# Kernel optimization log

Measured on AMD Instinct MI355X. Metric: run time of the kernel, lower is better.

Reference implementation:

```python
import jax, jax.numpy as jnp
import numpy as np
import math

D_MODEL = 512
NUM_HEADS = 8
B, S = 2, 4096


def setup_inputs() -> dict:
    key = jax.random.key(0)
    ks = jax.random.split(key, 11)
    d = D_MODEL
    sc = 1.0 / math.sqrt(d)
    return {
        "query": jax.random.normal(ks[0], (B, S, d), jnp.float32),
        "key": jax.random.normal(ks[1], (B, S, d), jnp.float32),
        "value": jax.random.normal(ks[2], (B, S, d), jnp.float32),
        "Wq": jax.random.normal(ks[3], (d, d), jnp.float32) * sc,
        "bq": jnp.zeros((d,), jnp.float32),
        "Wk": jax.random.normal(ks[4], (d, d), jnp.float32) * sc,
        "bk": jnp.zeros((d,), jnp.float32),
        "Wv": jax.random.normal(ks[5], (d, d), jnp.float32) * sc,
        "bv": jnp.zeros((d,), jnp.float32),
        "Wo": jax.random.normal(ks[6], (d, d), jnp.float32) * sc,
        "bo": jnp.zeros((d,), jnp.float32),
    }


def reference(query, key, value, Wq, bq, Wk, bk, Wv, bv, Wo, bo):
    b, q_len, d_model = query.shape
    k_len = key.shape[1]
    h = NUM_HEADS
    d_k = d_model // h
    q = (query @ Wq.T + bq).reshape(b, q_len, h, d_k)
    k = (key @ Wk.T + bk).reshape(b, k_len, h, d_k)
    v = (value @ Wv.T + bv).reshape(b, k_len, h, d_k)
    # NOTE: faithful to source — softmax WITHOUT pre-scaling, then divide by sqrt(d_k)
    comp = jnp.einsum('bqhd,bkhd->bhqk', q, k)
    attn = jax.nn.softmax(comp, axis=-1) / jnp.sqrt(jnp.asarray(d_k, comp.dtype))
    x = jnp.einsum('bhqk,bkhd->bqhd', attn, v)
    return x.reshape(b, q_len, d_model) @ Wo.T + bo
```

## Files before the change

kernel.cpp:

```cpp
#include <hip/hip_runtime.h>

typedef _Float16 f16;
typedef __fp16 fp16x2 __attribute__((ext_vector_type(2)));
typedef _Float16 half4 __attribute__((ext_vector_type(4)));
typedef _Float16 half8 __attribute__((ext_vector_type(8)));
typedef float f32x4 __attribute__((ext_vector_type(4)));
typedef float float4v __attribute__((ext_vector_type(4)));
typedef float float2v __attribute__((ext_vector_type(2)));

#define LOG2E 1.44269504088896340736f

__device__ __forceinline__ half8 cat8(half4 a, half4 b) {
    half8 r;
    r[0] = a[0]; r[1] = a[1]; r[2] = a[2]; r[3] = a[3];
    r[4] = b[0]; r[5] = b[1]; r[6] = b[2]; r[7] = b[3];
    return r;
}

union H8 { fp16x2 h2[4]; half8 h8; };

#define TR8(baddr, d0,d1,d2,d3,d4,d5,d6,d7)                                   \
  asm volatile("ds_read_b64_tr_b16 %0, %8 offset:0\n\t"                       \
               "ds_read_b64_tr_b16 %1, %8 offset:512\n\t"                     \
               "ds_read_b64_tr_b16 %2, %8 offset:128\n\t"                     \
               "ds_read_b64_tr_b16 %3, %8 offset:640\n\t"                     \
               "ds_read_b64_tr_b16 %4, %8 offset:256\n\t"                     \
               "ds_read_b64_tr_b16 %5, %8 offset:768\n\t"                     \
               "ds_read_b64_tr_b16 %6, %8 offset:384\n\t"                     \
               "ds_read_b64_tr_b16 %7, %8 offset:896"                         \
               : "=&v"(d0),"=&v"(d1),"=&v"(d2),"=&v"(d3),                     \
                 "=&v"(d4),"=&v"(d5),"=&v"(d6),"=&v"(d7)                      \
               : "v"(baddr) : "memory")

#define LGKM0_FENCE()                                                          \
  do { asm volatile("s_waitcnt lgkmcnt(0)" ::: "memory");                      \
       __builtin_amdgcn_sched_barrier(0); } while (0)

__device__ __forceinline__ float rowmax16(const f32x4 sf[4]) {
    float a = fmaxf(fmaxf(sf[0][0], sf[0][1]), fmaxf(sf[0][2], sf[0][3]));
    float b = fmaxf(fmaxf(sf[1][0], sf[1][1]), fmaxf(sf[1][2], sf[1][3]));
    float c = fmaxf(fmaxf(sf[2][0], sf[2][1]), fmaxf(sf[2][2], sf[2][3]));
    float d = fmaxf(fmaxf(sf[3][0], sf[3][1]), fmaxf(sf[3][2], sf[3][3]));
    return fmaxf(fmaxf(a, b), fmaxf(c, d));
}

__device__ __forceinline__ void max_defer(
    const f32x4 sf[4], float& mL, f32x4 o[4], f32x4& la)
{
    float vm = rowmax16(sf);
    vm = fmaxf(vm, __shfl_xor(vm, 16, 64));
    vm = fmaxf(vm, __shfl_xor(vm, 32, 64));
    float vmL = vm * LOG2E;
    if (__any(vmL > mL + 8.0f)) {
        float mn = fmaxf(mL, vmL);
        float al = __builtin_amdgcn_exp2f(mL - mn);
        la *= al;
        #pragma unroll
        for (int db = 0; db < 4; ++db) o[db] *= al;
        mL = mn;
    }
}

__device__ __forceinline__ void exp_pack(
    const f32x4 sf[4], float mL, H8& pb0, H8& pb1)
{
    float pe[16];
    #pragma unroll
    for (int kb = 0; kb < 4; ++kb)
        #pragma unroll
        for (int ro = 0; ro < 4; ++ro)
            pe[kb * 4 + ro] = __builtin_amdgcn_exp2f(fmaf(sf[kb][ro], LOG2E, -mL));
    pb0.h2[0] = __builtin_amdgcn_cvt_pkrtz(pe[0],  pe[1]);
    pb0.h2[1] = __builtin_amdgcn_cvt_pkrtz(pe[2],  pe[3]);
    pb0.h2[2] = __builtin_amdgcn_cvt_pkrtz(pe[4],  pe[5]);
    pb0.h2[3] = __builtin_amdgcn_cvt_pkrtz(pe[6],  pe[7]);
    pb1.h2[0] = __builtin_amdgcn_cvt_pkrtz(pe[8],  pe[9]);
    pb1.h2[1] = __builtin_amdgcn_cvt_pkrtz(pe[10], pe[11]);
    pb1.h2[2] = __builtin_amdgcn_cvt_pkrtz(pe[12], pe[13]);
    pb1.h2[3] = __builtin_amdgcn_cvt_pkrtz(pe[14], pe[15]);
}

__global__ __launch_bounds__(256) void qkv_proj(
    const float* __restrict__ Aq, const float* __restrict__ Ak, const float* __restrict__ Av,
    const float* __restrict__ Wq, const float* __restrict__ Wk, const float* __restrict__ Wv,
    const float* __restrict__ bq, const float* __restrict__ bk, const float* __restrict__ bv,
    f16* __restrict__ Qh, f16* __restrict__ Kh, f16* __restrict__ Vh)
{
    const int z = blockIdx.z;
    const float* __restrict__ A    = (z == 0) ? Aq : (z == 1) ? Ak : Av;
    const float* __restrict__ W    = (z == 0) ? Wq : (z == 1) ? Wk : Wv;
    const float* __restrict__ bias = (z == 0) ? bq : (z == 1) ? bk : bv;
    f16* __restrict__ dst          = (z == 0) ? Qh : (z == 1) ? Kh : Vh;

    __shared__ __align__(16) f16 As[128 * 40];
    __shared__ __align__(16) f16 Ws[128 * 40];

    const int t  = threadIdx.x;
    const int m0 = blockIdx.y * 128;
    const int n0 = blockIdx.x * 128;
    const int w = t >> 6, lane = t & 63, lr = lane & 15, lg = lane >> 4;
    const int wr = w >> 1, wc = w & 1;

    f32x4 acc[4][4] = {};

    for (int k0 = 0; k0 < 512; k0 += 32) {
        #pragma unroll
        for (int it = 0; it < 2; ++it) {
            int c = t + it * 256;
            int row  = c >> 2;
            int col8 = (c & 3) * 8;

            const float* ga = A + (size_t)(m0 + row) * 512 + k0 + col8;
            float4v a0 = *(const float4v*)ga;
            float4v a1 = *(const float4v*)(ga + 4);
            half8 ha;
            ha[0] = (f16)a0[0]; ha[1] = (f16)a0[1]; ha[2] = (f16)a0[2]; ha[3] = (f16)a0[3];
            ha[4] = (f16)a1[0]; ha[5] = (f16)a1[1]; ha[6] = (f16)a1[2]; ha[7] = (f16)a1[3];
            *(half8*)&As[row * 40 + col8] = ha;

            const float* gw = W + (size_t)(n0 + row) * 512 + k0 + col8;
            float4v w0 = *(const float4v*)gw;
            float4v w1 = *(const float4v*)(gw + 4);
            half8 hw;
            hw[0] = (f16)w0[0]; hw[1] = (f16)w0[1]; hw[2] = (f16)w0[2]; hw[3] = (f16)w0[3];
            hw[4] = (f16)w1[0]; hw[5] = (f16)w1[1]; hw[6] = (f16)w1[2]; hw[7] = (f16)w1[3];
            *(half8*)&Ws[row * 40 + col8] = hw;
        }
        __syncthreads();

        half8 af[4], bf[4];
        #pragma unroll
        for (int i = 0; i < 4; ++i) {
            af[i] = *(const half8*)&As[(wr * 64 + i * 16 + lr) * 40 + lg * 8];
            bf[i] = *(const half8*)&Ws[(wc * 64 + i * 16 + lr) * 40 + lg * 8];
        }
        #pragma unroll
        for (int mi = 0; mi < 4; ++mi)
            #pragma unroll
            for (int ni = 0; ni < 4; ++ni)
                acc[mi][ni] = __builtin_amdgcn_mfma_f32_16x16x32_f16(af[mi], bf[ni], acc[mi][ni], 0, 0, 0);
        __syncthreads();
    }

    #pragma unroll
    for (int mi = 0; mi < 4; ++mi) {
        #pragma unroll
        for (int ni = 0; ni < 4; ++ni) {
            int col = n0 + wc * 64 + ni * 16 + lr;
            float bv_ = bias[col];
            int h  = col >> 6;
            int dd = col & 63;
            #pragma unroll
            for (int r = 0; r < 4; ++r) {
                int row = m0 + wr * 64 + mi * 16 + lg * 4 + r;
                int b = row >> 12;
                int s = row & 4095;
                dst[(((size_t)(b * 8 + h)) * 4096 + s) * 64 + dd] = (f16)(acc[mi][ni][r] + bv_);
            }
        }
    }
}

__global__ __launch_bounds__(256, 2) void flash_attn(
    const f16* __restrict__ Qh, const f16* __restrict__ Kh, const f16* __restrict__ Vh,
    f16* __restrict__ Xp, float2v* __restrict__ mlp)
{
    const int bh  = blockIdx.y;
    const int z   = blockIdx.z;
    const int t = threadIdx.x, w = t >> 6, lane = t & 63, lr = lane & 15, lg = lane >> 4;
    const int q0 = blockIdx.x * 128 + w * 32;

    __shared__ __align__(16) f16 Ks[2][64 * 72];
    __shared__ __align__(16) f16 Vs[2][64 * 64];

    const size_t hb = (size_t)bh * (4096 * 64);

    half8 aq00 = *(const half8*)&Qh[hb + (size_t)(q0 + lr) * 64 + lg * 8];
    half8 aq01 = *(const half8*)&Qh[hb + (size_t)(q0 + lr) * 64 + 32 + lg * 8];
    half8 aq10 = *(const half8*)&Qh[hb + (size_t)(q0 + 16 + lr) * 64 + lg * 8];
    half8 aq11 = *(const half8*)&Qh[hb + (size_t)(q0 + 16 + lr) * 64 + 32 + lg * 8];

    half8 ones;
    #pragma unroll
    for (int j = 0; j < 8; ++j) ones[j] = (f16)1.0f;
    const f32x4 zf = {0.0f, 0.0f, 0.0f, 0.0f};

    const int srow = t >> 3;
    const int scol = (t & 7) * 8;
    const int kdstA = srow * 72 + scol;
    const int kdstB = kdstA + 32 * 72;
    const int vdstA = ((((srow >> 2) & 3) * 16) + (srow >> 4) * 4 + (scol >> 4)) * 64
                    + (srow & 3) * 16 + (scol & 15);
    const int vdstB = vdstA + 512;

    f32x4 o0[4] = {}, o1[4] = {};
    f32x4 la0 = {}, la1 = {};
    float mL0 = -INFINITY, mL1 = -INFINITY;

    const f16* kbase = Kh + hb + (size_t)(z * 2048 + srow) * 64 + scol;
    const f16* vbase = Vh + hb + (size_t)(z * 2048 + srow) * 64 + scol;

    half8 kregA = *(const half8*)kbase;
    half8 kregB = *(const half8*)(kbase + 2048);
    half8 vregA = *(const half8*)vbase;
    half8 vregB = *(const half8*)(vbase + 2048);

    for (int kt = 0; kt < 2048; kt += 64) {
        const int bi = (kt >> 6) & 1;
        f16* ks = &Ks[bi][0];
        f16* vs = &Vs[bi][0];

        *(half8*)&ks[kdstA] = kregA;
        *(half8*)&ks[kdstB] = kregB;
        *(half8*)&vs[vdstA] = vregA;
        *(half8*)&vs[vdstB] = vregB;
        __syncthreads();

        int koff = ((kt + 64) & 2047) << 6;
        kregA = *(const half8*)(kbase + koff);
        kregB = *(const half8*)(kbase + 2048 + koff);
        vregA = *(const half8*)(vbase + koff);
        vregB = *(const half8*)(vbase + 2048 + koff);

        f32x4 sf0[4], sf1[4];
        {
            half8 kf[4];
            #pragma unroll
            for (int kb = 0; kb < 4; ++kb)
                kf[kb] = *(const half8*)&ks[(kb * 16 + lr) * 72 + lg * 8];
            __builtin_amdgcn_s_setprio(1);
            #pragma unroll
            for (int kb = 0; kb < 4; ++kb)
                sf0[kb] = __builtin_amdgcn_mfma_f32_16x16x32_f16(kf[kb], aq00, zf, 0, 0, 0);
            #pragma unroll
            for (int kb = 0; kb < 4; ++kb)
                sf1[kb] = __builtin_amdgcn_mfma_f32_16x16x32_f16(kf[kb], aq10, zf, 0, 0, 0);
            __builtin_amdgcn_s_setprio(0);
            #pragma unroll
            for (int kb = 0; kb < 4; ++kb)
                kf[kb] = *(const half8*)&ks[(kb * 16 + lr) * 72 + 32 + lg * 8];
            __builtin_amdgcn_s_setprio(1);
            #pragma unroll
            for (int kb = 0; kb < 4; ++kb)
                sf0[kb] = __builtin_amdgcn_mfma_f32_16x16x32_f16(kf[kb], aq01, sf0[kb], 0, 0, 0);
            #pragma unroll
            for (int kb = 0; kb < 4; ++kb)
                sf1[kb] = __builtin_amdgcn_mfma_f32_16x16x32_f16(kf[kb], aq11, sf1[kb], 0, 0, 0);
            __builtin_amdgcn_s_setprio(0);
        }

        max_defer(sf0, mL0, o0, la0);
        max_defer(sf1, mL1, o1, la1);

        const unsigned vb = (unsigned)(size_t)vs + (unsigned)(lg * 2048 + lr * 8);
        half4 ua0,ua1,ua2,ua3,ua4,ua5,ua6,ua7;
        half4 ub0,ub1,ub2,ub3,ub4,ub5,ub6,ub7;
        TR8(vb,         ua0,ua1,ua2,ua3,ua4,ua5,ua6,ua7);
        TR8(vb + 1024u, ub0,ub1,ub2,ub3,ub4,ub5,ub6,ub7);

        H8 p00, p01, p10, p11;
        exp_pack(sf0, mL0, p00, p01);
        exp_pack(sf1, mL1, p10, p11);

        LGKM0_FENCE();

        __builtin_amdgcn_s_setprio(1);
        o0[0] = __builtin_amdgcn_mfma_f32_16x16x32_f16(cat8(ua0,ua1), p00.h8, o0[0], 0, 0, 0);
        o0[1] = __builtin_amdgcn_mfma_f32_16x16x32_f16(cat8(ua2,ua3), p00.h8, o0[1], 0, 0, 0);
        o0[2] = __builtin_amdgcn_mfma_f32_16x16x32_f16(cat8(ua4,ua5), p00.h8, o0[2], 0, 0, 0);
        o0[3] = __builtin_amdgcn_mfma_f32_16x16x32_f16(cat8(ua6,ua7), p00.h8, o0[3], 0, 0, 0);
        o1[0] = __builtin_amdgcn_mfma_f32_16x16x32_f16(cat8(ua0,ua1), p10.h8, o1[0], 0, 0, 0);
        o1[1] = __builtin_amdgcn_mfma_f32_16x16x32_f16(cat8(ua2,ua3), p10.h8, o1[1], 0, 0, 0);
        o1[2] = __builtin_amdgcn_mfma_f32_16x16x32_f16(cat8(ua4,ua5), p10.h8, o1[2], 0, 0, 0);
        o1[3] = __builtin_amdgcn_mfma_f32_16x16x32_f16(cat8(ua6,ua7), p10.h8, o1[3], 0, 0, 0);
        la0 = __builtin_amdgcn_mfma_f32_16x16x32_f16(ones, p00.h8, la0, 0, 0, 0);
        la1 = __builtin_amdgcn_mfma_f32_16x16x32_f16(ones, p10.h8, la1, 0, 0, 0);
        o0[0] = __builtin_amdgcn_mfma_f32_16x16x32_f16(cat8(ub0,ub1), p01.h8, o0[0], 0, 0, 0);
        o0[1] = __builtin_amdgcn_mfma_f32_16x16x32_f16(cat8(ub2,ub3), p01.h8, o0[1], 0, 0, 0);
        o0[2] = __builtin_amdgcn_mfma_f32_16x16x32_f16(cat8(ub4,ub5), p01.h8, o0[2], 0, 0, 0);
        o0[3] = __builtin_amdgcn_mfma_f32_16x16x32_f16(cat8(ub6,ub7), p01.h8, o0[3], 0, 0, 0);
        o1[0] = __builtin_amdgcn_mfma_f32_16x16x32_f16(cat8(ub0,ub1), p11.h8, o1[0], 0, 0, 0);
        o1[1] = __builtin_amdgcn_mfma_f32_16x16x32_f16(cat8(ub2,ub3), p11.h8, o1[1], 0, 0, 0);
        o1[2] = __builtin_amdgcn_mfma_f32_16x16x32_f16(cat8(ub4,ub5), p11.h8, o1[2], 0, 0, 0);
        o1[3] = __builtin_amdgcn_mfma_f32_16x16x32_f16(cat8(ub6,ub7), p11.h8, o1[3], 0, 0, 0);
        la0 = __builtin_amdgcn_mfma_f32_16x16x32_f16(ones, p01.h8, la0, 0, 0, 0);
        la1 = __builtin_amdgcn_mfma_f32_16x16x32_f16(ones, p11.h8, la1, 0, 0, 0);
        __builtin_amdgcn_s_setprio(0);
    }

    const int b = bh >> 3, h = bh & 7;
    f16* X = Xp + (size_t)z * (8192 * 512);
    const float inv0 = 1.0f / la0[0];
    const float inv1 = 1.0f / la1[0];
    const int q0_ = q0 + lr, q1_ = q0 + 16 + lr;
    #pragma unroll
    for (int db = 0; db < 4; ++db) {
        half4 hv0, hv1;
        hv0[0] = (f16)(o0[db][0] * inv0);
        hv0[1] = (f16)(o0[db][1] * inv0);
        hv0[2] = (f16)(o0[db][2] * inv0);
        hv0[3] = (f16)(o0[db][3] * inv0);
        *(half4*)&X[((size_t)(b * 4096 + q0_)) * 512 + h * 64 + db * 16 + lg * 4] = hv0;
        hv1[0] = (f16)(o1[db][0] * inv1);
        hv1[1] = (f16)(o1[db][1] * inv1);
        hv1[2] = (f16)(o1[db][2] * inv1);
        hv1[3] = (f16)(o1[db][3] * inv1);
        *(half4*)&X[((size_t)(b * 4096 + q1_)) * 512 + h * 64 + db * 16 + lg * 4] = hv1;
    }

    if (lane < 16) {
        float2v m0v; m0v[0] = mL0; m0v[1] = la0[0];
        float2v m1v; m1v[0] = mL1; m1v[1] = la1[0];
        mlp[(size_t)z * 65536 + bh * 4096 + q0_] = m0v;
        mlp[(size_t)z * 65536 + bh * 4096 + q1_] = m1v;
    }
}

__global__ __launch_bounds__(256) void out_proj(
    const f16* __restrict__ Xp, const float2v* __restrict__ mlp,
    const float* __restrict__ Wo, const float* __restrict__ bo,
    float* __restrict__ out)
{
    __shared__ __align__(16) f16 As[128 * 40];
    __shared__ __align__(16) f16 Ws[128 * 40];

    const int t  = threadIdx.x;
    const int m0 = blockIdx.y * 128;
    const int n0 = blockIdx.x * 128;
    const int w = t >> 6, lane = t & 63, lr = lane & 15, lg = lane >> 4;
    const int wr = w >> 1, wc = w & 1;

    f32x4 acc[4][4] = {};

    for (int k0 = 0; k0 < 512; k0 += 32) {
        #pragma unroll
        for (int it = 0; it < 2; ++it) {
            int c = t + it * 256;
            int row  = c >> 2;
            int col8 = (c & 3) * 8;
            int gcol = k0 + col8;
            int tok  = m0 + row;

            int bhq = ((tok >> 12) * 8 + (gcol >> 6)) * 4096 + (tok & 4095);
            float2v ml1 = mlp[bhq];
            float2v ml2 = mlp[65536 + bhq];
            float mm = fmaxf(ml1[0], ml2[0]);
            float a1 = __builtin_amdgcn_exp2f(ml1[0] - mm) * ml1[1];
            float a2 = __builtin_amdgcn_exp2f(ml2[0] - mm) * ml2[1];
            float inv = 1.0f / (8.0f * (a1 + a2));
            float w1 = a1 * inv, w2 = a2 * inv;

            const size_t xoff = (size_t)tok * 512 + gcol;
            half8 x1 = *(const half8*)&Xp[xoff];
            half8 x2 = *(const half8*)&Xp[(size_t)8192 * 512 + xoff];
            half8 hx;
            #pragma unroll
            for (int j = 0; j < 8; ++j)
                hx[j] = (f16)(w1 * (float)x1[j] + w2 * (float)x2[j]);
            *(half8*)&As[row * 40 + col8] = hx;

            const float* gw = Wo + (size_t)(n0 + row) * 512 + k0 + col8;
            float4v w0 = *(const float4v*)gw;
            float4v w1v = *(const float4v*)(gw + 4);
            half8 hw;
            hw[0] = (f16)w0[0];  hw[1] = (f16)w0[1];  hw[2] = (f16)w0[2];  hw[3] = (f16)w0[3];
            hw[4] = (f16)w1v[0]; hw[5] = (f16)w1v[1]; hw[6] = (f16)w1v[2]; hw[7] = (f16)w1v[3];
            *(half8*)&Ws[row * 40 + col8] = hw;
        }
        __syncthreads();

        half8 af[4], bf[4];
        #pragma unroll
        for (int i = 0; i < 4; ++i) {
            af[i] = *(const half8*)&As[(wr * 64 + i * 16 + lr) * 40 + lg * 8];
            bf[i] = *(const half8*)&Ws[(wc * 64 + i * 16 + lr) * 40 + lg * 8];
        }
        #pragma unroll
        for (int mi = 0; mi < 4; ++mi)
            #pragma unroll
            for (int ni = 0; ni < 4; ++ni)
                acc[mi][ni] = __builtin_amdgcn_mfma_f32_16x16x32_f16(af[mi], bf[ni], acc[mi][ni], 0, 0, 0);
        __syncthreads();
    }

    #pragma unroll
    for (int mi = 0; mi < 4; ++mi) {
        #pragma unroll
        for (int ni = 0; ni < 4; ++ni) {
            int col = n0 + wc * 64 + ni * 16 + lr;
            float bb = bo[col];
            #pragma unroll
            for (int r = 0; r < 4; ++r) {
                int row = m0 + wr * 64 + mi * 16 + lg * 4 + r;
                out[(size_t)row * 512 + col] = acc[mi][ni][r] + bb;
            }
        }
    }
}

extern "C" void kernel_launch(void* const* d_in, const int* in_sizes, int n_in,
                              void* d_out, int out_size, void* d_ws, size_t ws_size,
                              hipStream_t stream) {
    const float* query = (const float*)d_in[0];
    const float* key   = (const float*)d_in[1];
    const float* value = (const float*)d_in[2];
    const float* Wq    = (const float*)d_in[3];
    const float* bq    = (const float*)d_in[4];
    const float* Wk    = (const float*)d_in[5];
    const float* bk    = (const float*)d_in[6];
    const float* Wv    = (const float*)d_in[7];
    const float* bv    = (const float*)d_in[8];
    const float* Wo    = (const float*)d_in[9];
    const float* bo    = (const float*)d_in[10];
    float* out = (float*)d_out;

    char* ws = (char*)d_ws;
    f16*     Qh  = (f16*)(ws);
    f16*     Kh  = (f16*)(ws + 8388608);
    f16*     Vh  = (f16*)(ws + 16777216);
    f16*     Xp  = (f16*)(ws + 25165824);
    float2v* mlp = (float2v*)(ws + 41943040);

    qkv_proj<<<dim3(4, 64, 3), 256, 0, stream>>>(query, key, value,
                                                 Wq, Wk, Wv, bq, bk, bv,
                                                 Qh, Kh, Vh);
    flash_attn<<<dim3(32, 16, 2), 256, 0, stream>>>(Qh, Kh, Vh, Xp, mlp);
    out_proj<<<dim3(4, 64), 256, 0, stream>>>(Xp, mlp, Wo, bo, out);
}
```

Before: 170.3 us.

## Store V transposed from projection and drop LDS transpose reads in attention

```diff
diff --git a/kernel.cpp b/kernel.cpp
--- a/kernel.cpp
+++ b/kernel.cpp
@@ -10,31 +10,8 @@
 
 #define LOG2E 1.44269504088896340736f
 
-__device__ __forceinline__ half8 cat8(half4 a, half4 b) {
-    half8 r;
-    r[0] = a[0]; r[1] = a[1]; r[2] = a[2]; r[3] = a[3];
-    r[4] = b[0]; r[5] = b[1]; r[6] = b[2]; r[7] = b[3];
-    return r;
-}
-
 union H8 { fp16x2 h2[4]; half8 h8; };
-
-#define TR8(baddr, d0,d1,d2,d3,d4,d5,d6,d7)                                   \
-  asm volatile("ds_read_b64_tr_b16 %0, %8 offset:0\n\t"                       \
-               "ds_read_b64_tr_b16 %1, %8 offset:512\n\t"                     \
-               "ds_read_b64_tr_b16 %2, %8 offset:128\n\t"                     \
-               "ds_read_b64_tr_b16 %3, %8 offset:640\n\t"                     \
-               "ds_read_b64_tr_b16 %4, %8 offset:256\n\t"                     \
-               "ds_read_b64_tr_b16 %5, %8 offset:768\n\t"                     \
-               "ds_read_b64_tr_b16 %6, %8 offset:384\n\t"                     \
-               "ds_read_b64_tr_b16 %7, %8 offset:896"                         \
-               : "=&v"(d0),"=&v"(d1),"=&v"(d2),"=&v"(d3),                     \
-                 "=&v"(d4),"=&v"(d5),"=&v"(d6),"=&v"(d7)                      \
-               : "v"(baddr) : "memory")
-
-#define LGKM0_FENCE()                                                          \
-  do { asm volatile("s_waitcnt lgkmcnt(0)" ::: "memory");                      \
-       __builtin_amdgcn_sched_barrier(0); } while (0)
+union HV { half8 h8; half4 h4[2]; };
 
 __device__ __forceinline__ float rowmax16(const f32x4 sf[4]) {
     float a = fmaxf(fmaxf(sf[0][0], sf[0][1]), fmaxf(sf[0][2], sf[0][3]));
@@ -84,13 +61,13 @@
     const float* __restrict__ Aq, const float* __restrict__ Ak, const float* __restrict__ Av,
     const float* __restrict__ Wq, const float* __restrict__ Wk, const float* __restrict__ Wv,
     const float* __restrict__ bq, const float* __restrict__ bk, const float* __restrict__ bv,
-    f16* __restrict__ Qh, f16* __restrict__ Kh, f16* __restrict__ Vh)
+    f16* __restrict__ Qh, f16* __restrict__ Kh, f16* __restrict__ Vt)
 {
     const int z = blockIdx.z;
     const float* __restrict__ A    = (z == 0) ? Aq : (z == 1) ? Ak : Av;
     const float* __restrict__ W    = (z == 0) ? Wq : (z == 1) ? Wk : Wv;
     const float* __restrict__ bias = (z == 0) ? bq : (z == 1) ? bk : bv;
-    f16* __restrict__ dst          = (z == 0) ? Qh : (z == 1) ? Kh : Vh;
+    f16* __restrict__ dst          = (z == 0) ? Qh : (z == 1) ? Kh : Vt;
 
     __shared__ __align__(16) f16 As[128 * 40];
     __shared__ __align__(16) f16 Ws[128 * 40];
@@ -142,27 +119,49 @@
         __syncthreads();
     }
 
-    #pragma unroll
-    for (int mi = 0; mi < 4; ++mi) {
-        #pragma unroll
-        for (int ni = 0; ni < 4; ++ni) {
-            int col = n0 + wc * 64 + ni * 16 + lr;
-            float bv_ = bias[col];
-            int h  = col >> 6;
-            int dd = col & 63;
-            #pragma unroll
-            for (int r = 0; r < 4; ++r) {
-                int row = m0 + wr * 64 + mi * 16 + lg * 4 + r;
-                int b = row >> 12;
-                int s = row & 4095;
-                dst[(((size_t)(b * 8 + h)) * 4096 + s) * 64 + dd] = (f16)(acc[mi][ni][r] + bv_);
+    if (z == 2) {
+        #pragma unroll
+        for (int mi = 0; mi < 4; ++mi) {
+            #pragma unroll
+            for (int ni = 0; ni < 4; ++ni) {
+                int col = n0 + wc * 64 + ni * 16 + lr;
+                float bv_ = bias[col];
+                int h  = col >> 6;
+                int dd = col & 63;
+                int row0 = m0 + wr * 64 + mi * 16 + lg * 4;
+                int b  = row0 >> 12;
+                int s0 = row0 & 4095;
+                half4 hv;
+                hv[0] = (f16)(acc[mi][ni][0] + bv_);
+                hv[1] = (f16)(acc[mi][ni][1] + bv_);
+                hv[2] = (f16)(acc[mi][ni][2] + bv_);
+                hv[3] = (f16)(acc[mi][ni][3] + bv_);
+                *(half4*)&dst[(((size_t)(b * 8 + h)) * 64 + dd) * 4096 + s0] = hv;
             }
         }
+    } else {
+        #pragma unroll
+        for (int mi = 0; mi < 4; ++mi) {
+            #pragma unroll
+            for (int ni = 0; ni < 4; ++ni) {
+                int col = n0 + wc * 64 + ni * 16 + lr;
+                float bv_ = bias[col];
+                int h  = col >> 6;
+                int dd = col & 63;
+                #pragma unroll
+                for (int r = 0; r < 4; ++r) {
+                    int row = m0 + wr * 64 + mi * 16 + lg * 4 + r;
+                    int b = row >> 12;
+                    int s = row & 4095;
+                    dst[(((size_t)(b * 8 + h)) * 4096 + s) * 64 + dd] = (f16)(acc[mi][ni][r] + bv_);
+                }
+            }
+        }
     }
 }
 
 __global__ __launch_bounds__(256, 2) void flash_attn(
-    const f16* __restrict__ Qh, const f16* __restrict__ Kh, const f16* __restrict__ Vh,
+    const f16* __restrict__ Qh, const f16* __restrict__ Kh, const f16* __restrict__ Vt,
     f16* __restrict__ Xp, float2v* __restrict__ mlp)
 {
     const int bh  = blockIdx.y;
@@ -171,7 +170,7 @@
     const int q0 = blockIdx.x * 128 + w * 32;
 
     __shared__ __align__(16) f16 Ks[2][64 * 72];
-    __shared__ __align__(16) f16 Vs[2][64 * 64];
+    __shared__ __align__(16) f16 Vs[2][64 * 72];
 
     const size_t hb = (size_t)bh * (4096 * 64);
 
@@ -186,24 +185,25 @@
     const f32x4 zf = {0.0f, 0.0f, 0.0f, 0.0f};
 
     const int srow = t >> 3;
-    const int scol = (t & 7) * 8;
+    const int u    = t & 7;
+    const int scol = u * 8;
     const int kdstA = srow * 72 + scol;
     const int kdstB = kdstA + 32 * 72;
-    const int vdstA = ((((srow >> 2) & 3) * 16) + (srow >> 4) * 4 + (scol >> 4)) * 64
-                    + (srow & 3) * 16 + (scol & 15);
-    const int vdstB = vdstA + 512;
+    const int vposb = ((u >> 2) & 1) * 32 + (u & 1) * 16 + ((u >> 1) & 1) * 4;
+    const int vdstA = srow * 72 + vposb;
+    const int vdstB = vdstA + 32 * 72;
 
     f32x4 o0[4] = {}, o1[4] = {};
     f32x4 la0 = {}, la1 = {};
     float mL0 = -INFINITY, mL1 = -INFINITY;
 
     const f16* kbase = Kh + hb + (size_t)(z * 2048 + srow) * 64 + scol;
-    const f16* vbase = Vh + hb + (size_t)(z * 2048 + srow) * 64 + scol;
+    const f16* vbase = Vt + hb + (size_t)srow * 4096 + z * 2048 + scol;
 
     half8 kregA = *(const half8*)kbase;
     half8 kregB = *(const half8*)(kbase + 2048);
     half8 vregA = *(const half8*)vbase;
-    half8 vregB = *(const half8*)(vbase + 2048);
+    half8 vregB = *(const half8*)(vbase + (size_t)32 * 4096);
 
     for (int kt = 0; kt < 2048; kt += 64) {
         const int bi = (kt >> 6) & 1;
@@ -212,15 +212,21 @@
 
         *(half8*)&ks[kdstA] = kregA;
         *(half8*)&ks[kdstB] = kregB;
-        *(half8*)&vs[vdstA] = vregA;
-        *(half8*)&vs[vdstB] = vregB;
+        {
+            HV a_; a_.h8 = vregA;
+            *(half4*)&vs[vdstA]     = a_.h4[0];
+            *(half4*)&vs[vdstA + 8] = a_.h4[1];
+            HV b_; b_.h8 = vregB;
+            *(half4*)&vs[vdstB]     = b_.h4[0];
+            *(half4*)&vs[vdstB + 8] = b_.h4[1];
+        }
         __syncthreads();
 
-        int koff = ((kt + 64) & 2047) << 6;
-        kregA = *(const half8*)(kbase + koff);
-        kregB = *(const half8*)(kbase + 2048 + koff);
+        int koff = ((kt + 64) & 2047);
+        kregA = *(const half8*)(kbase + (size_t)koff * 64);
+        kregB = *(const half8*)(kbase + 2048 + (size_t)koff * 64);
         vregA = *(const half8*)(vbase + koff);
-        vregB = *(const half8*)(vbase + 2048 + koff);
+        vregB = *(const half8*)(vbase + (size_t)32 * 4096 + koff);
 
         f32x4 sf0[4], sf1[4];
         {
@@ -252,37 +258,36 @@
         max_defer(sf0, mL0, o0, la0);
         max_defer(sf1, mL1, o1, la1);
 
-        const unsigned vb = (unsigned)(size_t)vs + (unsigned)(lg * 2048 + lr * 8);
-        half4 ua0,ua1,ua2,ua3,ua4,ua5,ua6,ua7;
-        half4 ub0,ub1,ub2,ub3,ub4,ub5,ub6,ub7;
-        TR8(vb,         ua0,ua1,ua2,ua3,ua4,ua5,ua6,ua7);
-        TR8(vb + 1024u, ub0,ub1,ub2,ub3,ub4,ub5,ub6,ub7);
+        half8 va[4], vb_[4];
+        #pragma unroll
+        for (int db = 0; db < 4; ++db) {
+            va[db]  = *(const half8*)&vs[(db * 16 + lr) * 72 + lg * 8];
+            vb_[db] = *(const half8*)&vs[(db * 16 + lr) * 72 + 32 + lg * 8];
+        }
 
         H8 p00, p01, p10, p11;
         exp_pack(sf0, mL0, p00, p01);
         exp_pack(sf1, mL1, p10, p11);
 
-        LGKM0_FENCE();
-
         __builtin_amdgcn_s_setprio(1);
-        o0[0] = __builtin_amdgcn_mfma_f32_16x16x32_f16(cat8(ua0,ua1), p00.h8, o0[0], 0, 0, 0);
-        o0[1] = __builtin_amdgcn_mfma_f32_16x16x32_f16(cat8(ua2,ua3), p00.h8, o0[1], 0, 0, 0);
-        o0[2] = __builtin_amdgcn_mfma_f32_16x16x32_f16(cat8(ua4,ua5), p00.h8, o0[2], 0, 0, 0);
-        o0[3] = __builtin_amdgcn_mfma_f32_16x16x32_f16(cat8(ua6,ua7), p00.h8, o0[3], 0, 0, 0);
-        o1[0] = __builtin_amdgcn_mfma_f32_16x16x32_f16(cat8(ua0,ua1), p10.h8, o1[0], 0, 0, 0);
-        o1[1] = __builtin_amdgcn_mfma_f32_16x16x32_f16(cat8(ua2,ua3), p10.h8, o1[1], 0, 0, 0);
-        o1[2] = __builtin_amdgcn_mfma_f32_16x16x32_f16(cat8(ua4,ua5), p10.h8, o1[2], 0, 0, 0);
-        o1[3] = __builtin_amdgcn_mfma_f32_16x16x32_f16(cat8(ua6,ua7), p10.h8, o1[3], 0, 0, 0);
+        o0[0] = __builtin_amdgcn_mfma_f32_16x16x32_f16(va[0], p00.h8, o0[0], 0, 0, 0);
+        o0[1] = __builtin_amdgcn_mfma_f32_16x16x32_f16(va[1], p00.h8, o0[1], 0, 0, 0);
+        o0[2] = __builtin_amdgcn_mfma_f32_16x16x32_f16(va[2], p00.h8, o0[2], 0, 0, 0);
+        o0[3] = __builtin_amdgcn_mfma_f32_16x16x32_f16(va[3], p00.h8, o0[3], 0, 0, 0);
+        o1[0] = __builtin_amdgcn_mfma_f32_16x16x32_f16(va[0], p10.h8, o1[0], 0, 0, 0);
+        o1[1] = __builtin_amdgcn_mfma_f32_16x16x32_f16(va[1], p10.h8, o1[1], 0, 0, 0);
+        o1[2] = __builtin_amdgcn_mfma_f32_16x16x32_f16(va[2], p10.h8, o1[2], 0, 0, 0);
+        o1[3] = __builtin_amdgcn_mfma_f32_16x16x32_f16(va[3], p10.h8, o1[3], 0, 0, 0);
         la0 = __builtin_amdgcn_mfma_f32_16x16x32_f16(ones, p00.h8, la0, 0, 0, 0);
         la1 = __builtin_amdgcn_mfma_f32_16x16x32_f16(ones, p10.h8, la1, 0, 0, 0);
-        o0[0] = __builtin_amdgcn_mfma_f32_16x16x32_f16(cat8(ub0,ub1), p01.h8, o0[0], 0, 0, 0);
-        o0[1] = __builtin_amdgcn_mfma_f32_16x16x32_f16(cat8(ub2,ub3), p01.h8, o0[1], 0, 0, 0);
-        o0[2] = __builtin_amdgcn_mfma_f32_16x16x32_f16(cat8(ub4,ub5), p01.h8, o0[2], 0, 0, 0);
-        o0[3] = __builtin_amdgcn_mfma_f32_16x16x32_f16(cat8(ub6,ub7), p01.h8, o0[3], 0, 0, 0);
-        o1[0] = __builtin_amdgcn_mfma_f32_16x16x32_f16(cat8(ub0,ub1), p11.h8, o1[0], 0, 0, 0);
-        o1[1] = __builtin_amdgcn_mfma_f32_16x16x32_f16(cat8(ub2,ub3), p11.h8, o1[1], 0, 0, 0);
-        o1[2] = __builtin_amdgcn_mfma_f32_16x16x32_f16(cat8(ub4,ub5), p11.h8, o1[2], 0, 0, 0);
-        o1[3] = __builtin_amdgcn_mfma_f32_16x16x32_f16(cat8(ub6,ub7), p11.h8, o1[3], 0, 0, 0);
+        o0[0] = __builtin_amdgcn_mfma_f32_16x16x32_f16(vb_[0], p01.h8, o0[0], 0, 0, 0);
+        o0[1] = __builtin_amdgcn_mfma_f32_16x16x32_f16(vb_[1], p01.h8, o0[1], 0, 0, 0);
+        o0[2] = __builtin_amdgcn_mfma_f32_16x16x32_f16(vb_[2], p01.h8, o0[2], 0, 0, 0);
+        o0[3] = __builtin_amdgcn_mfma_f32_16x16x32_f16(vb_[3], p01.h8, o0[3], 0, 0, 0);
+        o1[0] = __builtin_amdgcn_mfma_f32_16x16x32_f16(vb_[0], p11.h8, o1[0], 0, 0, 0);
+        o1[1] = __builtin_amdgcn_mfma_f32_16x16x32_f16(vb_[1], p11.h8, o1[1], 0, 0, 0);
+        o1[2] = __builtin_amdgcn_mfma_f32_16x16x32_f16(vb_[2], p11.h8, o1[2], 0, 0, 0);
+        o1[3] = __builtin_amdgcn_mfma_f32_16x16x32_f16(vb_[3], p11.h8, o1[3], 0, 0, 0);
         la0 = __builtin_amdgcn_mfma_f32_16x16x32_f16(ones, p01.h8, la0, 0, 0, 0);
         la1 = __builtin_amdgcn_mfma_f32_16x16x32_f16(ones, p11.h8, la1, 0, 0, 0);
         __builtin_amdgcn_s_setprio(0);
@@ -417,13 +422,13 @@
     char* ws = (char*)d_ws;
     f16*     Qh  = (f16*)(ws);
     f16*     Kh  = (f16*)(ws + 8388608);
-    f16*     Vh  = (f16*)(ws + 16777216);
+    f16*     Vt  = (f16*)(ws + 16777216);
     f16*     Xp  = (f16*)(ws + 25165824);
     float2v* mlp = (float2v*)(ws + 41943040);
 
     qkv_proj<<<dim3(4, 64, 3), 256, 0, stream>>>(query, key, value,
                                                  Wq, Wk, Wv, bq, bk, bv,
-                                                 Qh, Kh, Vh);
-    flash_attn<<<dim3(32, 16, 2), 256, 0, stream>>>(Qh, Kh, Vh, Xp, mlp);
+                                                 Qh, Kh, Vt);
+    flash_attn<<<dim3(32, 16, 2), 256, 0, stream>>>(Qh, Kh, Vt, Xp, mlp);
     out_proj<<<dim3(4, 64), 256, 0, stream>>>(Xp, mlp, Wo, bo, out);
 }
```

New measurement: 170.4 us. No clear change (+0.0%).
